# Kernel tuning notes

Hardware: AMD Instinct MI355X
Metric: run time of the kernel (lower is better)

Reference implementation:

```python
import jax, jax.numpy as jnp
import numpy as np

DIM = 1024
HEADS = 8
DIM_HEAD = 64
HIDDEN = HEADS * DIM_HEAD  # 512
SCALE = DIM_HEAD ** -0.5
BATCH = 16384
EPS = 1e-12  # F.normalize eps


def setup_inputs() -> dict:
    key = jax.random.key(0)
    k0, k1, k2 = jax.random.split(key, 3)
    x = jax.random.normal(k0, (BATCH, DIM), dtype=jnp.float32)
    w_qkv = jax.random.normal(k1, (3 * HIDDEN, DIM), dtype=jnp.float32) * 0.02
    w_out = jax.random.normal(k2, (DIM, HIDDEN), dtype=jnp.float32) * 0.02
    b_out = jnp.zeros((DIM,), dtype=jnp.float32)
    g = jnp.ones((1, DIM), dtype=jnp.float32)
    return {"x": x, "w_qkv": w_qkv, "w_out": w_out, "b_out": b_out, "g": g}


def reference(x, w_qkv, w_out, b_out, g):
    b = x.shape[0]
    # Conv1d(kernel=1, no bias) on n=1 sequence == matmul with (3*hidden, dim) weight
    qkv = x @ w_qkv.T  # (b, 3*hidden)
    q, k, v = jnp.split(qkv, 3, axis=1)  # each (b, hidden)
    # rearrange 'b (h c) n -> b h c n' with n=1 -> (b, h, c)
    q = q.reshape(b, HEADS, DIM_HEAD)
    k = k.reshape(b, HEADS, DIM_HEAD)
    v = v.reshape(b, HEADS, DIM_HEAD)
    # q.softmax(dim=-2) is over the c axis
    q = jax.nn.softmax(q, axis=-1) * SCALE
    # k.softmax(dim=-1) is over the n axis of size 1 -> all ones (kept faithful)
    k = jax.nn.softmax(k[..., None], axis=-1)[..., 0]
    # context = einsum('bhdn,bhen->bhde', k, v); out = einsum('bhde,bhdn->bhen', context, q)
    # with n=1 this collapses to out_e = (sum_d k_d q_d) * v_e; fused to avoid (b,h,d,e)
    s = jnp.einsum('bhd,bhd->bh', k, q)  # (b, h)
    out = s[..., None] * v  # (b, h, e)
    out = out.reshape(b, HIDDEN)  # 'b h c n -> b (h c) n', squeeze(-1)
    # Linear(hidden, dim)
    out = out @ w_out.T + b_out  # (b, dim)
    # RMSNorm_MLP: F.normalize(x, dim=1) * g * sqrt(dim)
    norm = jnp.linalg.norm(out, axis=1, keepdims=True)
    out = out / jnp.maximum(norm, EPS) * g * jnp.sqrt(jnp.float32(DIM))
    return out
```

## Files before the change

kernel.cpp:

```cpp
#include <hip/hip_runtime.h>
#include <hip/hip_bf16.h>


typedef __attribute__((ext_vector_type(8))) short bf16x8;
typedef __attribute__((ext_vector_type(4))) float f32x4;

struct alignas(16) bfvec8 { __hip_bfloat16 h[8]; };

__device__ __forceinline__ bfvec8 pack8(float4 a, float4 b) {
    bfvec8 o;
    o.h[0] = __float2bfloat16(a.x); o.h[1] = __float2bfloat16(a.y);
    o.h[2] = __float2bfloat16(a.z); o.h[3] = __float2bfloat16(a.w);
    o.h[4] = __float2bfloat16(b.x); o.h[5] = __float2bfloat16(b.y);
    o.h[6] = __float2bfloat16(b.z); o.h[7] = __float2bfloat16(b.w);
    return o;
}

__global__ __launch_bounds__(256)
void prep(const float* __restrict__ Wo, const float* __restrict__ Wv,
          __hip_bfloat16* __restrict__ Weff,
          const float* __restrict__ X, __hip_bfloat16* __restrict__ Xbf) {
    __shared__ __align__(16) __hip_bfloat16 As[64 * 32];
    __shared__ __align__(16) __hip_bfloat16 Bs[64 * 32];
    __shared__ __align__(16) float Bf[32 * 65];

    const int tid = threadIdx.x;

    if (blockIdx.x >= 256) {
        const size_t nv = (size_t)16384 * 1024 / 8;
        const size_t stride = (size_t)2048 * 256;
        for (size_t i = (size_t)(blockIdx.x - 256) * 256 + tid; i < nv; i += stride) {
            const float4 a = *(const float4*)(X + i * 8);
            const float4 b = *(const float4*)(X + i * 8 + 4);
            *(bfvec8*)(Xbf + i * 8) = pack8(a, b);
        }
        return;
    }

    const int lane = tid & 63;
    const int wave = tid >> 6;
    const int wm   = wave >> 1;
    const int wn   = wave & 1;
    const int quad = lane >> 4;
    const int tr   = lane & 15;
    const int m0   = (blockIdx.x >> 4) * 64;
    const int n0   = (blockIdx.x & 15) * 64;

    f32x4 acc[2][2];
#pragma unroll
    for (int i = 0; i < 2; ++i)
#pragma unroll
        for (int j = 0; j < 2; ++j)
            acc[i][j] = (f32x4){0.f, 0.f, 0.f, 0.f};

    for (int kt = 0; kt < 512; kt += 32) {
        {
            int r = tid >> 2, c = tid & 3;
            int s = (r >> 1) & 3;
            int kg = (c ^ s) << 3;
            const float* sp = Wo + (size_t)(m0 + r) * 512 + kt + kg;
            float4 a = *(const float4*)sp, b = *(const float4*)(sp + 4);
            *(bfvec8*)(As + r * 32 + (c << 3)) = pack8(a, b);
        }
        {
            int kr = tid >> 3, c8 = (tid & 7) << 3;
            const float* sp = Wv + (size_t)(kt + kr) * 1024 + n0 + c8;
            float4 a = *(const float4*)sp, b = *(const float4*)(sp + 4);
            *(float4*)(Bf + kr * 65 + c8)     = a;
            *(float4*)(Bf + kr * 65 + c8 + 4) = b;
        }
        __syncthreads();
        {
            int n = tid >> 2, cc = tid & 3, k8 = cc << 3;
            float4 a, b;
            a.x = Bf[(k8 + 0) * 65 + n]; a.y = Bf[(k8 + 1) * 65 + n];
            a.z = Bf[(k8 + 2) * 65 + n]; a.w = Bf[(k8 + 3) * 65 + n];
            b.x = Bf[(k8 + 4) * 65 + n]; b.y = Bf[(k8 + 5) * 65 + n];
            b.z = Bf[(k8 + 6) * 65 + n]; b.w = Bf[(k8 + 7) * 65 + n];
            int cs = cc ^ ((n >> 1) & 3);
            *(bfvec8*)(Bs + n * 32 + cs * 8) = pack8(a, b);
        }
        __syncthreads();

        bf16x8 af[2], bfr[2];
#pragma unroll
        for (int mi = 0; mi < 2; ++mi) {
            int r = wm * 32 + mi * 16 + tr;
            int c = quad ^ ((r >> 1) & 3);
            af[mi] = *(const bf16x8*)(As + r * 32 + c * 8);
        }
#pragma unroll
        for (int ni = 0; ni < 2; ++ni) {
            int r = wn * 32 + ni * 16 + tr;
            int c = quad ^ ((r >> 1) & 3);
            bfr[ni] = *(const bf16x8*)(Bs + r * 32 + c * 8);
        }
#pragma unroll
        for (int mi = 0; mi < 2; ++mi)
#pragma unroll
            for (int ni = 0; ni < 2; ++ni)
                acc[mi][ni] = __builtin_amdgcn_mfma_f32_16x16x32_bf16(
                    af[mi], bfr[ni], acc[mi][ni], 0, 0, 0);
        __syncthreads();
    }

#pragma unroll
    for (int mi = 0; mi < 2; ++mi)
#pragma unroll
        for (int ni = 0; ni < 2; ++ni) {
            const int col = n0 + wn * 32 + ni * 16 + tr;
#pragma unroll
            for (int r = 0; r < 4; ++r) {
                const int row = m0 + wm * 32 + mi * 16 + quad * 4 + r;
                Weff[(size_t)row * 1024 + col] =
                    __float2bfloat16(acc[mi][ni][r] * 0.125f);
            }
        }
}


#define GLL(gp, lp) __builtin_amdgcn_global_load_lds( \
    (const __attribute__((address_space(1))) void*)(gp), \
    (__attribute__((address_space(3))) void*)(lp), 16, 0, 0)

#define STAGE_A(BUF, H, U) do { \
    GLL(Xbf + Ab0 + (size_t)(H) * 131072 + (size_t)(U) * 64, \
        sm + (BUF) * 32768 + (H) * 8192 + ldsA);             \
    GLL(Xbf + Ab1 + (size_t)(H) * 131072 + (size_t)(U) * 64, \
        sm + (BUF) * 32768 + (H) * 8192 + 4096 + ldsA);      \
} while (0)

#define STAGE_B(BUF, H, U) do { \
    GLL(Bt + Bb0 + (size_t)(H) * 131072 + (size_t)(U) * 64,  \
        sm + (BUF) * 32768 + 16384 + (H) * 8192 + ldsA);     \
    GLL(Bt + Bb1 + (size_t)(H) * 131072 + (size_t)(U) * 64,  \
        sm + (BUF) * 32768 + 16384 + (H) * 8192 + 4096 + ldsA); \
} while (0)

__global__ __launch_bounds__(512, 2)
void main_gemm(const __hip_bfloat16* __restrict__ Xbf,
               const __hip_bfloat16* __restrict__ Bt,
               const float* __restrict__ bias,
               __hip_bfloat16* __restrict__ Y) {
    __shared__ __align__(16) __hip_bfloat16 sm[2 * 32768];

    const int tid  = threadIdx.x;
    const int lane = tid & 63;
    const int wc   = tid >> 6;
    const int quad = lane >> 4;
    const int tr   = lane & 15;
    const int rlow = tr & 7;

    const int xcd  = blockIdx.x & 7;
    const int orig = xcd * 32 + (blockIdx.x >> 3);
    const int m0   = (orig >> 2) * 256;
    const int n0   = (orig & 3) * 256;

    const int r0 = tid >> 3,            c0 = tid & 7;
    const int r1 = (tid + 512) >> 3,    c1 = tid & 7;
    const size_t Ab0 = (size_t)(m0 + r0) * 1024 + ((c0 ^ (r0 & 7)) << 3);
    const size_t Ab1 = (size_t)(m0 + r1) * 1024 + ((c1 ^ (r1 & 7)) << 3);
    const size_t Bb0 = (size_t)(n0 + r0) * 1024 + ((c0 ^ (r0 & 7)) << 3);
    const size_t Bb1 = (size_t)(n0 + r1) * 1024 + ((c1 ^ (r1 & 7)) << 3);
    const int ldsA = tid * 8;

    int ac[2];
#pragma unroll
    for (int ko = 0; ko < 2; ++ko) ac[ko] = ((ko * 4 + quad) ^ rlow) * 8;
    const int rdA = tr * 64;
    const int rdB = wc * 2048 + tr * 64;

    f32x4 acc[16][2];
#pragma unroll
    for (int f = 0; f < 16; ++f)
#pragma unroll
        for (int ni = 0; ni < 2; ++ni)
            acc[f][ni] = (f32x4){0.f, 0.f, 0.f, 0.f};

    STAGE_B(0, 0, 0); STAGE_B(0, 1, 0); STAGE_A(0, 0, 0); STAGE_A(0, 1, 0);
    STAGE_B(1, 0, 1); STAGE_B(1, 1, 1); STAGE_A(1, 0, 1);
    asm volatile("s_waitcnt vmcnt(6)" ::: "memory");
    __builtin_amdgcn_s_barrier();

    bf16x8 bfr[2][2];

    for (int it = 0; it < 8; ++it) {
#pragma unroll
        for (int rb = 0; rb < 2; ++rb) {
            const int u = it * 2 + rb;
#pragma unroll
            for (int ph = 0; ph < 2; ++ph) {
                bf16x8 af[4][2];
#pragma unroll
                for (int mi = 0; mi < 4; ++mi)
#pragma unroll
                    for (int ko = 0; ko < 2; ++ko)
                        af[mi][ko] = *(const bf16x8*)(
                            sm + rb * 32768 + (ph * 2) * 4096 + mi * 1024 + rdA + ac[ko]);
                if (ph == 0) {
#pragma unroll
                    for (int ni = 0; ni < 2; ++ni)
#pragma unroll
                        for (int ko = 0; ko < 2; ++ko)
                            bfr[ni][ko] = *(const bf16x8*)(
                                sm + rb * 32768 + 16384 + rdB + ni * 1024 + ac[ko]);
                }

                if (ph == 0) {
                    if (u + 1 < 16) STAGE_A(rb ^ 1, 1, u + 1);
                } else {
                    if (u + 2 < 16) {
                        STAGE_B(rb, 0, u + 2);
                        STAGE_B(rb, 1, u + 2);
                        STAGE_A(rb, 0, u + 2);
                    }
                }

                __builtin_amdgcn_s_barrier();
                asm volatile("s_waitcnt lgkmcnt(0)" ::: "memory");
                __builtin_amdgcn_sched_barrier(0);

                __builtin_amdgcn_s_setprio(1);
#pragma unroll
                for (int mi = 0; mi < 4; ++mi)
#pragma unroll
                    for (int ni = 0; ni < 2; ++ni)
#pragma unroll
                        for (int ko = 0; ko < 2; ++ko)
                            acc[ph * 8 + mi][ni] = __builtin_amdgcn_mfma_f32_16x16x32_bf16(
                                af[mi][ko], bfr[ni][ko], acc[ph * 8 + mi][ni], 0, 0, 0);
                __builtin_amdgcn_s_setprio(0);

                bf16x8 ag[4][2];
#pragma unroll
                for (int mi = 0; mi < 4; ++mi)
#pragma unroll
                    for (int ko = 0; ko < 2; ++ko)
                        ag[mi][ko] = *(const bf16x8*)(
                            sm + rb * 32768 + (ph * 2 + 1) * 4096 + mi * 1024 + rdA + ac[ko]);

                __builtin_amdgcn_s_setprio(1);
#pragma unroll
                for (int mi = 0; mi < 4; ++mi)
#pragma unroll
                    for (int ni = 0; ni < 2; ++ni)
#pragma unroll
                        for (int ko = 0; ko < 2; ++ko)
                            acc[ph * 8 + 4 + mi][ni] = __builtin_amdgcn_mfma_f32_16x16x32_bf16(
                                ag[mi][ko], bfr[ni][ko], acc[ph * 8 + 4 + mi][ni], 0, 0, 0);
                __builtin_amdgcn_s_setprio(0);

                if (ph == 1) {
                    if (u <= 13)      asm volatile("s_waitcnt vmcnt(6)" ::: "memory");
                    else if (u == 14) asm volatile("s_waitcnt vmcnt(0)" ::: "memory");
                    if (u < 15) __builtin_amdgcn_s_barrier();
                } else {
                    __builtin_amdgcn_s_barrier();
                }
            }
        }
    }

    float bv[2]; int col[2];
#pragma unroll
    for (int ni = 0; ni < 2; ++ni) {
        col[ni] = n0 + wc * 32 + ni * 16 + tr;
        bv[ni]  = bias[col[ni]];
    }
#pragma unroll
    for (int f = 0; f < 16; ++f)
#pragma unroll
        for (int ni = 0; ni < 2; ++ni)
#pragma unroll
            for (int rr = 0; rr < 4; ++rr) {
                const int row = m0 + f * 16 + quad * 4 + rr;
                Y[(size_t)row * 1024 + col[ni]] =
                    __float2bfloat16(acc[f][ni][rr] + bv[ni]);
            }
}

__global__ __launch_bounds__(256)
void rmsnorm2(const __hip_bfloat16* __restrict__ y, const float* __restrict__ g,
              float* __restrict__ out) {
    const int wave = threadIdx.x >> 6;
    const int sub  = wave >> 1;
    const int t    = threadIdx.x & 127;
    const int row  = blockIdx.x * 2 + sub;
    const size_t base = (size_t)row * 1024 + t * 8;

    union { uint4 u; ushort s[8]; } U;
    U.u = *(const uint4*)(y + base);
    float v[8];
#pragma unroll
    for (int j = 0; j < 8; ++j)
        v[j] = __bfloat162float(*(const __hip_bfloat16*)&U.s[j]);

    float ss = 0.f;
#pragma unroll
    for (int j = 0; j < 8; ++j) ss += v[j] * v[j];
#pragma unroll
    for (int off = 32; off > 0; off >>= 1)
        ss += __shfl_down(ss, off, 64);

    __shared__ float wsum[4];
    if ((threadIdx.x & 63) == 0) wsum[wave] = ss;
    __syncthreads();
    const float total = wsum[sub * 2] + wsum[sub * 2 + 1];
    const float sc = 32.0f / fmaxf(sqrtf(total), 1e-12f);

    const float4 g0 = *(const float4*)(g + t * 8);
    const float4 g1 = *(const float4*)(g + t * 8 + 4);
    float4 o0, o1;
    o0.x = v[0] * sc * g0.x; o0.y = v[1] * sc * g0.y;
    o0.z = v[2] * sc * g0.z; o0.w = v[3] * sc * g0.w;
    o1.x = v[4] * sc * g1.x; o1.y = v[5] * sc * g1.y;
    o1.z = v[6] * sc * g1.z; o1.w = v[7] * sc * g1.w;
    *(float4*)(out + base)     = o0;
    *(float4*)(out + base + 4) = o1;
}

extern "C" void kernel_launch(void* const* d_in, const int* in_sizes, int n_in,
                              void* d_out, int out_size, void* d_ws, size_t ws_size,
                              hipStream_t stream) {
    const float* x     = (const float*)d_in[0];
    const float* w_qkv = (const float*)d_in[1];
    const float* w_out = (const float*)d_in[2];
    const float* b_out = (const float*)d_in[3];
    const float* g     = (const float*)d_in[4];

    const int B = 16384, D = 1024, H = 512;
    const float* wv = w_qkv + (size_t)2 * H * D;

    char* ws = (char*)d_ws;
    size_t off = 0;
    __hip_bfloat16* weff_bf = (__hip_bfloat16*)(ws + off); off += (size_t)D * D * 2;
    __hip_bfloat16* y_bf    = (__hip_bfloat16*)(ws + off); off += (size_t)B * D * 2;
    __hip_bfloat16* x_bf    = (__hip_bfloat16*)(ws + off); off += (size_t)B * D * 2;

    prep<<<256 + 2048, 256, 0, stream>>>(w_out, wv, weff_bf, x, x_bf);
    main_gemm<<<256, 512, 0, stream>>>(x_bf, weff_bf, b_out, y_bf);
    rmsnorm2<<<B / 2, 256, 0, stream>>>(y_bf, g, (float*)d_out);
}
```

Measured before the change: 177.2 us.

## Remap GEMM waves to a 2x4 grid with 128x64 per-wave tiles

Changes the main GEMM wave layout from 8 waves each covering 256 rows by 32 columns to a 2x4 wave grid where each wave covers 128 rows by 64 columns. This lowers LDS read traffic per MFMA, since each wave loads fewer A fragments relative to B. Each k-step now runs two phases instead of four, and the global-to-LDS staging is regrouped into per-quarter loads. It also changes barrier placement and the vmcnt accounting, which could expose latency or risk a mismatch in the prefetch counts.

```diff
diff --git a/kernel.cpp b/kernel.cpp
--- a/kernel.cpp
+++ b/kernel.cpp
@@ -123,19 +123,13 @@
     (const __attribute__((address_space(1))) void*)(gp), \
     (__attribute__((address_space(3))) void*)(lp), 16, 0, 0)
 
-#define STAGE_A(BUF, H, U) do { \
-    GLL(Xbf + Ab0 + (size_t)(H) * 131072 + (size_t)(U) * 64, \
-        sm + (BUF) * 32768 + (H) * 8192 + ldsA);             \
-    GLL(Xbf + Ab1 + (size_t)(H) * 131072 + (size_t)(U) * 64, \
-        sm + (BUF) * 32768 + (H) * 8192 + 4096 + ldsA);      \
-} while (0)
-
-#define STAGE_B(BUF, H, U) do { \
-    GLL(Bt + Bb0 + (size_t)(H) * 131072 + (size_t)(U) * 64,  \
-        sm + (BUF) * 32768 + 16384 + (H) * 8192 + ldsA);     \
-    GLL(Bt + Bb1 + (size_t)(H) * 131072 + (size_t)(U) * 64,  \
-        sm + (BUF) * 32768 + 16384 + (H) * 8192 + 4096 + ldsA); \
-} while (0)
+#define STAGE_AQ(BUF, Q, U) \
+    GLL(Xbf + Abase + (size_t)(Q) * 65536 + (size_t)(U) * 64, \
+        sm + (BUF) * 32768 + (Q) * 4096 + tid * 8)
+
+#define STAGE_BQ(BUF, Q, U) \
+    GLL(Bt + Bbase + (size_t)(Q) * 65536 + (size_t)(U) * 64, \
+        sm + (BUF) * 32768 + 16384 + (Q) * 4096 + tid * 8)
 
 __global__ __launch_bounds__(512, 2)
 void main_gemm(const __hip_bfloat16* __restrict__ Xbf,
@@ -146,7 +140,9 @@
 
     const int tid  = threadIdx.x;
     const int lane = tid & 63;
-    const int wc   = tid >> 6;
+    const int w    = tid >> 6;
+    const int wr   = w >> 2;
+    const int wn   = w & 3;
     const int quad = lane >> 4;
     const int tr   = lane & 15;
     const int rlow = tr & 7;
@@ -156,124 +152,118 @@
     const int m0   = (orig >> 2) * 256;
     const int n0   = (orig & 3) * 256;
 
-    const int r0 = tid >> 3,            c0 = tid & 7;
-    const int r1 = (tid + 512) >> 3,    c1 = tid & 7;
-    const size_t Ab0 = (size_t)(m0 + r0) * 1024 + ((c0 ^ (r0 & 7)) << 3);
-    const size_t Ab1 = (size_t)(m0 + r1) * 1024 + ((c1 ^ (r1 & 7)) << 3);
-    const size_t Bb0 = (size_t)(n0 + r0) * 1024 + ((c0 ^ (r0 & 7)) << 3);
-    const size_t Bb1 = (size_t)(n0 + r1) * 1024 + ((c1 ^ (r1 & 7)) << 3);
-    const int ldsA = tid * 8;
+    const int sr = tid >> 3, scn = tid & 7;
+    const int kg = ((scn ^ (sr & 7)) << 3);
+    const size_t Abase = (size_t)(m0 + sr) * 1024 + kg;
+    const size_t Bbase = (size_t)(n0 + sr) * 1024 + kg;
 
     int ac[2];
 #pragma unroll
     for (int ko = 0; ko < 2; ++ko) ac[ko] = ((ko * 4 + quad) ^ rlow) * 8;
     const int rdA = tr * 64;
-    const int rdB = wc * 2048 + tr * 64;
-
-    f32x4 acc[16][2];
-#pragma unroll
-    for (int f = 0; f < 16; ++f)
-#pragma unroll
-        for (int ni = 0; ni < 2; ++ni)
+    const int rdB = 16384 + wn * 4096 + tr * 64;
+
+    f32x4 acc[8][4];
+#pragma unroll
+    for (int f = 0; f < 8; ++f)
+#pragma unroll
+        for (int ni = 0; ni < 4; ++ni)
             acc[f][ni] = (f32x4){0.f, 0.f, 0.f, 0.f};
 
-    STAGE_B(0, 0, 0); STAGE_B(0, 1, 0); STAGE_A(0, 0, 0); STAGE_A(0, 1, 0);
-    STAGE_B(1, 0, 1); STAGE_B(1, 1, 1); STAGE_A(1, 0, 1);
+    STAGE_AQ(0, 0, 0); STAGE_AQ(0, 1, 0); STAGE_AQ(0, 2, 0); STAGE_AQ(0, 3, 0);
+    STAGE_BQ(0, 0, 0); STAGE_BQ(0, 1, 0); STAGE_BQ(0, 2, 0); STAGE_BQ(0, 3, 0);
+    STAGE_BQ(1, 0, 1); STAGE_BQ(1, 1, 1); STAGE_BQ(1, 2, 1); STAGE_BQ(1, 3, 1);
+    STAGE_AQ(1, 0, 1); STAGE_AQ(1, 2, 1);
     asm volatile("s_waitcnt vmcnt(6)" ::: "memory");
     __builtin_amdgcn_s_barrier();
 
-    bf16x8 bfr[2][2];
+    bf16x8 bfr[4][2];
 
     for (int it = 0; it < 8; ++it) {
 #pragma unroll
         for (int rb = 0; rb < 2; ++rb) {
             const int u = it * 2 + rb;
-#pragma unroll
-            for (int ph = 0; ph < 2; ++ph) {
-                bf16x8 af[4][2];
-#pragma unroll
-                for (int mi = 0; mi < 4; ++mi)
+
+            bf16x8 af[4][2];
+#pragma unroll
+            for (int mi = 0; mi < 4; ++mi)
+#pragma unroll
+                for (int ko = 0; ko < 2; ++ko)
+                    af[mi][ko] = *(const bf16x8*)(
+                        sm + rb * 32768 + (wr * 2) * 4096 + mi * 1024 + rdA + ac[ko]);
+#pragma unroll
+            for (int ni = 0; ni < 4; ++ni)
+#pragma unroll
+                for (int ko = 0; ko < 2; ++ko)
+                    bfr[ni][ko] = *(const bf16x8*)(
+                        sm + rb * 32768 + rdB + ni * 1024 + ac[ko]);
+
+            if (u + 1 < 16) { STAGE_AQ(rb ^ 1, 1, u + 1); STAGE_AQ(rb ^ 1, 3, u + 1); }
+
+            __builtin_amdgcn_s_barrier();
+            asm volatile("s_waitcnt lgkmcnt(0)" ::: "memory");
+            __builtin_amdgcn_sched_barrier(0);
+
+            __builtin_amdgcn_s_setprio(1);
+#pragma unroll
+            for (int mi = 0; mi < 4; ++mi)
+#pragma unroll
+                for (int ni = 0; ni < 4; ++ni)
 #pragma unroll
                     for (int ko = 0; ko < 2; ++ko)
-                        af[mi][ko] = *(const bf16x8*)(
-                            sm + rb * 32768 + (ph * 2) * 4096 + mi * 1024 + rdA + ac[ko]);
-                if (ph == 0) {
-#pragma unroll
-                    for (int ni = 0; ni < 2; ++ni)
-#pragma unroll
-                        for (int ko = 0; ko < 2; ++ko)
-                            bfr[ni][ko] = *(const bf16x8*)(
-                                sm + rb * 32768 + 16384 + rdB + ni * 1024 + ac[ko]);
-                }
-
-                if (ph == 0) {
-                    if (u + 1 < 16) STAGE_A(rb ^ 1, 1, u + 1);
-                } else {
-                    if (u + 2 < 16) {
-                        STAGE_B(rb, 0, u + 2);
-                        STAGE_B(rb, 1, u + 2);
-                        STAGE_A(rb, 0, u + 2);
-                    }
-                }
-
-                __builtin_amdgcn_s_barrier();
-                asm volatile("s_waitcnt lgkmcnt(0)" ::: "memory");
-                __builtin_amdgcn_sched_barrier(0);
-
-                __builtin_amdgcn_s_setprio(1);
-#pragma unroll
-                for (int mi = 0; mi < 4; ++mi)
-#pragma unroll
-                    for (int ni = 0; ni < 2; ++ni)
-#pragma unroll
-                        for (int ko = 0; ko < 2; ++ko)
-                            acc[ph * 8 + mi][ni] = __builtin_amdgcn_mfma_f32_16x16x32_bf16(
-                                af[mi][ko], bfr[ni][ko], acc[ph * 8 + mi][ni], 0, 0, 0);
-                __builtin_amdgcn_s_setprio(0);
-
-                bf16x8 ag[4][2];
-#pragma unroll
-                for (int mi = 0; mi < 4; ++mi)
+                        acc[mi][ni] = __builtin_amdgcn_mfma_f32_16x16x32_bf16(
+                            af[mi][ko], bfr[ni][ko], acc[mi][ni], 0, 0, 0);
+            __builtin_amdgcn_s_setprio(0);
+            __builtin_amdgcn_s_barrier();
+
+#pragma unroll
+            for (int mi = 0; mi < 4; ++mi)
+#pragma unroll
+                for (int ko = 0; ko < 2; ++ko)
+                    af[mi][ko] = *(const bf16x8*)(
+                        sm + rb * 32768 + (wr * 2 + 1) * 4096 + mi * 1024 + rdA + ac[ko]);
+
+            if (u + 2 < 16) {
+                STAGE_BQ(rb, 0, u + 2); STAGE_BQ(rb, 1, u + 2);
+                STAGE_BQ(rb, 2, u + 2); STAGE_BQ(rb, 3, u + 2);
+                STAGE_AQ(rb, 0, u + 2); STAGE_AQ(rb, 2, u + 2);
+            }
+
+            __builtin_amdgcn_s_barrier();
+            asm volatile("s_waitcnt lgkmcnt(0)" ::: "memory");
+            __builtin_amdgcn_sched_barrier(0);
+
+            __builtin_amdgcn_s_setprio(1);
+#pragma unroll
+            for (int mi = 0; mi < 4; ++mi)
+#pragma unroll
+                for (int ni = 0; ni < 4; ++ni)
 #pragma unroll
                     for (int ko = 0; ko < 2; ++ko)
-                        ag[mi][ko] = *(const bf16x8*)(
-                            sm + rb * 32768 + (ph * 2 + 1) * 4096 + mi * 1024 + rdA + ac[ko]);
-
-                __builtin_amdgcn_s_setprio(1);
-#pragma unroll
-                for (int mi = 0; mi < 4; ++mi)
-#pragma unroll
-                    for (int ni = 0; ni < 2; ++ni)
-#pragma unroll
-                        for (int ko = 0; ko < 2; ++ko)
-                            acc[ph * 8 + 4 + mi][ni] = __builtin_amdgcn_mfma_f32_16x16x32_bf16(
-                                ag[mi][ko], bfr[ni][ko], acc[ph * 8 + 4 + mi][ni], 0, 0, 0);
-                __builtin_amdgcn_s_setprio(0);
-
-                if (ph == 1) {
-                    if (u <= 13)      asm volatile("s_waitcnt vmcnt(6)" ::: "memory");
-                    else if (u == 14) asm volatile("s_waitcnt vmcnt(0)" ::: "memory");
-                    if (u < 15) __builtin_amdgcn_s_barrier();
-                } else {
-                    __builtin_amdgcn_s_barrier();
-                }
-            }
+                        acc[4 + mi][ni] = __builtin_amdgcn_mfma_f32_16x16x32_bf16(
+                            af[mi][ko], bfr[ni][ko], acc[4 + mi][ni], 0, 0, 0);
+            __builtin_amdgcn_s_setprio(0);
+
+            if (u <= 13)      asm volatile("s_waitcnt vmcnt(6)" ::: "memory");
+            else if (u == 14) asm volatile("s_waitcnt vmcnt(0)" ::: "memory");
+            if (u < 15) __builtin_amdgcn_s_barrier();
         }
     }
 
-    float bv[2]; int col[2];
-#pragma unroll
-    for (int ni = 0; ni < 2; ++ni) {
-        col[ni] = n0 + wc * 32 + ni * 16 + tr;
+    float bv[4]; int col[4];
+#pragma unroll
+    for (int ni = 0; ni < 4; ++ni) {
+        col[ni] = n0 + wn * 64 + ni * 16 + tr;
         bv[ni]  = bias[col[ni]];
     }
 #pragma unroll
-    for (int f = 0; f < 16; ++f)
-#pragma unroll
-        for (int ni = 0; ni < 2; ++ni)
+    for (int f = 0; f < 8; ++f)
+#pragma unroll
+        for (int ni = 0; ni < 4; ++ni)
 #pragma unroll
             for (int rr = 0; rr < 4; ++rr) {
-                const int row = m0 + f * 16 + quad * 4 + rr;
+                const int row = m0 + wr * 128 + (f >> 2) * 64 + (f & 3) * 16
+                              + quad * 4 + rr;
                 Y[(size_t)row * 1024 + col[ni]] =
                     __float2bfloat16(acc[f][ni][rr] + bv[ni]);
             }
```

Result: no change. 175.3 us (-1.1%).
